# Performance work log

Hardware: AMD Instinct MI355X
Metric: run time of the kernel (lower is better)

## Reference

```python
import jax, jax.numpy as jnp
import numpy as np

C = 256   # num_channels
H = 16    # num_heads
L = 16384 # protein length
W = 15    # window (odd -> same-length conv with pad=(W-1)//2)


def setup_inputs() -> dict:
    key = jax.random.key(0)
    k = jax.random.split(key, 5)
    x = jax.random.normal(k[0], (1, C, L), dtype=jnp.float32)
    w_heads = jax.random.normal(k[1], (H, C, W), dtype=jnp.float32) * (1.0 / np.sqrt(C * W))
    b_heads = jax.random.normal(k[2], (H,), dtype=jnp.float32) * 0.01
    # grouped 1x1 conv with groups=H: per-head [C_out, C_in] matrices
    w_tr = jax.random.normal(k[3], (H, C, C), dtype=jnp.float32) * (1.0 / np.sqrt(C))
    b_tr = jax.random.normal(k[4], (H, C), dtype=jnp.float32) * 0.01
    return {"x": x, "w_heads": w_heads, "b_heads": b_heads, "w_tr": w_tr, "b_tr": b_tr}


def reference(x, w_heads, b_heads, w_tr, b_tr):
    pad = (W - 1) // 2
    # conv_heads: Conv1d(C -> H, kernel W, pad (W-1)//2)  -> scores [1, H, L]
    scores = jax.lax.conv_general_dilated(
        x, w_heads, window_strides=(1,), padding=[(pad, pad)],
        dimension_numbers=("NCH", "OIH", "NCH"),
    ) + b_heads[None, :, None]
    # batchwise softmax over sequence (single protein in batch -> softmax over L)
    focuses = jax.nn.softmax(scores, axis=-1)  # [1, H, L]
    # outer product: [1, H, 1, L] * [1, 1, C, L] -> [1, H, C, L] (the big intermediate)
    focused = focuses[:, :, None, :] * x[:, None, :, :]
    # grouped 1x1 conv (per-head CxC matmul) then sum over heads -> [1, C, L]
    out = jnp.einsum("hoc,bhcl->bol", w_tr, focused)
    out = out + jnp.sum(b_tr, axis=0)[None, :, None]  # head-summed per-group bias
    return out
```

## Files before the change

kernel.cpp:

```cpp
#include <hip/hip_runtime.h>
#include <hip/hip_bf16.h>

#define L_LEN 16384
#define C_CH  256
#define H_HEADS 16
#define W_WIN 15

typedef __attribute__((ext_vector_type(8))) short bf16x8;
typedef __attribute__((ext_vector_type(4))) float f32x4;
typedef unsigned short ushort_t;


__device__ __forceinline__ void gll16(const void* g, void* l) {
    __builtin_amdgcn_global_load_lds(
        (const __attribute__((address_space(1))) void*)g,
        (__attribute__((address_space(3))) void*)l, 16, 0, 0);
}

__device__ __forceinline__ ushort_t f2bf(float f) {
    __hip_bfloat16 b = __float2bfloat16(f);
    return *(ushort_t*)&b;
}

__global__ __launch_bounds__(256) void k_prep(const float* __restrict__ x,
                                              const float* __restrict__ wtr,
                                              const float* __restrict__ wh,
                                              ushort_t* __restrict__ xb,
                                              ushort_t* __restrict__ Ag,
                                              ushort_t* __restrict__ awf) {
    int bid = blockIdx.x;
    int t = threadIdx.x;
    if (bid < 1024) {
        __shared__ float tile[64][65];
        int l0 = (bid & 255) * 64;
        int c0 = (bid >> 8) * 64;
#pragma unroll
        for (int r = 0; r < 16; ++r) {
            int c = r * 4 + (t >> 6);
            int l = t & 63;
            tile[c][l] = x[(size_t)(c0 + c) * L_LEN + l0 + l];
        }
        __syncthreads();
        int l = t >> 2;
        int cq = (t & 3) * 16;
        ushort_t tmp[16];
#pragma unroll
        for (int i = 0; i < 16; ++i) tmp[i] = f2bf(tile[cq + i][l]);
        char* rowp = (char*)(xb + (size_t)(l0 + l) * C_CH);
        int swz = (l & 7) << 4;
        int b0 = (c0 + cq) * 2;
        *(uint4*)(rowp + (b0 ^ swz)) = *(uint4*)&tmp[0];
        *(uint4*)(rowp + ((b0 + 16) ^ swz)) = *(uint4*)&tmp[8];
    } else if (bid < 1536) {
        int tid = (bid - 1024) * 256 + t;
        size_t D = (size_t)tid * 16;
        int m = (int)(D >> 13);
        int inner = (int)(D & 8191);
        int kt = inner >> 7, wb = inner & 127;
        int ob = kt * 128 + (wb ^ ((m & 7) << 4));
        int k0 = ob >> 1;
        int h = k0 >> 8, c = k0 & 255;
        const float* src = wtr + ((size_t)h * C_CH + m) * C_CH + c;
        ushort_t tmp[8];
#pragma unroll
        for (int i = 0; i < 8; ++i) tmp[i] = f2bf(src[i]);
        *(uint4*)((char*)Ag + D) = *(uint4*)tmp;
    } else {
        int tid = (bid - 1536) * 256 + t;
        int e = tid & 7;
        int lane = (tid >> 3) & 63;
        int ktw = tid >> 9;
        int w = ktw >> 3, kt = ktw & 7;
        int h = lane & 15;
        int c = kt * 32 + (lane >> 4) * 8 + e;
        awf[tid] = f2bf(wh[((size_t)h * C_CH + c) * W_WIN + w]);
    }
}

__global__ __launch_bounds__(128) void k_convm(const ushort_t* __restrict__ xb,
                                               const ushort_t* __restrict__ awf,
                                               float* __restrict__ scores) {
    __shared__ char xs[48 * 512];
    int t = threadIdx.x;
    int n0 = blockIdx.x * 32;
#pragma unroll
    for (int i = 0; i < 12; ++i) {
        int chunk = t + i * 128;
        int rr = chunk >> 5;
        int cb = (chunk & 31) * 16;
        int l = n0 - 8 + rr;
        int lc = l < 0 ? 0 : (l >= L_LEN ? L_LEN - 1 : l);
        gll16((const char*)xb + (size_t)lc * 512 + cb, xs + chunk * 16);
    }
    __syncthreads();
    if (n0 == 0 || n0 == L_LEN - 32) {
        int rbase = (n0 == 0) ? 0 : 40;
        uint4 z = {0u, 0u, 0u, 0u};
#pragma unroll
        for (int i = 0; i < 2; ++i) {
            int ch = t + i * 128;
            *(uint4*)(xs + rbase * 512 + ch * 16) = z;
        }
        __syncthreads();
    }
    int wv = t >> 6, lane = t & 63;
    int r = lane & 15, q = lane >> 4;
    const f32x4 vzero = {0.f, 0.f, 0.f, 0.f};
    f32x4 acc[4] = {vzero, vzero, vzero, vzero};
    for (int w = 0; w < 15; ++w) {
        int rr = wv * 16 + r + w + 1;
        const char* rowp = &xs[rr * 512];
        int sw = (rr & 7) << 4;
#pragma unroll
        for (int kt = 0; kt < 8; ++kt) {
            bf16x8 a = *(const bf16x8*)(awf + (size_t)(((w * 8 + kt) * 64 + lane) * 8));
            bf16x8 b = *(const bf16x8*)(rowp + ((kt * 64 + q * 16) ^ sw));
            acc[kt & 3] = __builtin_amdgcn_mfma_f32_16x16x32_bf16(a, b, acc[kt & 3], 0, 0, 0);
        }
    }
    f32x4 s = acc[0] + acc[1] + acc[2] + acc[3];
    int nb = n0 + wv * 16;
#pragma unroll
    for (int e = 0; e < 4; ++e)
        scores[(size_t)(q * 4 + e) * L_LEN + nb + r] = s[e];
}

__global__ __launch_bounds__(1024) void k_stats(const float* __restrict__ scores,
                                                const float* __restrict__ btr,
                                                float2* __restrict__ MZ,
                                                float* __restrict__ bias) {
    int t = threadIdx.x;
    if (blockIdx.x == 16) {
        if (t < 256) {
            float s = 0.f;
#pragma unroll
            for (int h = 0; h < H_HEADS; ++h) s += btr[h * C_CH + t];
            bias[t] = s;
        }
        return;
    }
    __shared__ float red[17];
    int h = blockIdx.x;
    int wid = t >> 6, ln = t & 63;
    const float* sp = scores + (size_t)h * L_LEN;
    float v[16];
    float mx = -1e30f;
#pragma unroll
    for (int i = 0; i < 16; ++i) {
        v[i] = sp[i * 1024 + t];
        mx = fmaxf(mx, v[i]);
    }
    for (int o = 32; o > 0; o >>= 1) mx = fmaxf(mx, __shfl_xor(mx, o));
    if (ln == 0) red[wid] = mx;
    __syncthreads();
    if (t == 0) {
        float m2 = red[0];
        for (int i = 1; i < 16; ++i) m2 = fmaxf(m2, red[i]);
        red[16] = m2;
    }
    __syncthreads();
    float M = red[16];
    float s = 0.f;
#pragma unroll
    for (int i = 0; i < 16; ++i) s += __expf(v[i] - M);
    for (int o = 32; o > 0; o >>= 1) s += __shfl_xor(s, o);
    __syncthreads();
    if (ln == 0) red[wid] = s;
    __syncthreads();
    if (t == 0) {
        float Z = 0.f;
        for (int i = 0; i < 16; ++i) Z += red[i];
        float2 r; r.x = M; r.y = 1.0f / Z;
        MZ[h] = r;
    }
}

#define BRES 65536
#define ATS  16384
#define FTAB (BRES + 4 * ATS)

__global__ __launch_bounds__(512, 1) void k_gemm(const ushort_t* __restrict__ Ag,
                                                 const ushort_t* __restrict__ xb,
                                                 const float* __restrict__ scores,
                                                 const float2* __restrict__ MZ,
                                                 const float* __restrict__ bias,
                                                 float* __restrict__ out) {
    __shared__ char lds[FTAB + 8192];
    int t = threadIdx.x;
    int w = t >> 6, lane = t & 63;
    int m0 = blockIdx.y * 128, n0 = blockIdx.x * 128;
    int wr = w >> 2, wc = w & 3;
    int r = lane & 15, q = lane >> 4;
    int swz = (r & 7) << 4;

#pragma unroll
    for (int i = 0; i < 8; ++i) {
        int chunk = t + i * 512;
        int row = chunk >> 5, cb = (chunk & 31) * 16;
        gll16((const char*)xb + (size_t)(n0 + row) * 512 + cb, lds + chunk * 16);
    }
    {
        int idx = t * 4;
        int hh = idx >> 7, nn = idx & 127;
        float2 mz = MZ[hh];
        const float* sp = scores + (size_t)hh * L_LEN + n0 + nn;
        float* ft = (float*)(lds + FTAB);
#pragma unroll
        for (int e = 0; e < 4; ++e)
            ft[idx + e] = __expf(sp[e] - mz.x) * mz.y;
    }
    const f32x4 vzero = {0.f, 0.f, 0.f, 0.f};
    f32x4 oacc[4][2], hacc[4][2];
#pragma unroll
    for (int i = 0; i < 4; ++i)
#pragma unroll
        for (int j = 0; j < 2; ++j) { oacc[i][j] = vzero; hacc[i][j] = vzero; }

    bf16x8 br00_0, br00_1, br01_0, br01_1, br10_0, br10_1, br11_0, br11_1,
           br20_0, br20_1, br21_0, br21_1, br30_0, br30_1, br31_0, br31_1;

    __syncthreads();

    auto stageA = [&](int buf, int kt) {
        const char* src = (const char*)Ag + (size_t)(m0 + (t >> 3)) * 8192 + kt * 128 + (t & 7) * 16;
        char* dst = lds + BRES + buf * ATS + t * 16;
#pragma unroll
        for (int j = 0; j < 2; ++j)
            gll16(src + (size_t)j * 64 * 8192, dst + j * 8192);
    };

#define BRN(QQ, KK, J) br##QQ##KK##_##J
#define LDB(QQ, KK, J)                                                            \
    BRN(QQ, KK, J) = *(const bf16x8*)(lds + (wc * 32 + (J) * 16 + r) * 512 +      \
                          (((QQ) * 128 + (KK) * 64 + q * 16) ^ swz))
#define LDA_(Ab, I, KK)                                                           \
    (*(const bf16x8*)((Ab) + (wr * 64 + (I) * 16 + r) * 128 +                     \
                      (((KK) * 64 + q * 16) ^ swz)))
#define CK(Ab, KK, B0, B1)                                                        \
    {                                                                             \
        bf16x8 a0 = LDA_(Ab, 0, KK), a1 = LDA_(Ab, 1, KK),                        \
               a2 = LDA_(Ab, 2, KK), a3 = LDA_(Ab, 3, KK);                        \
        hacc[0][0] = __builtin_amdgcn_mfma_f32_16x16x32_bf16(a0, B0, hacc[0][0], 0, 0, 0); \
        hacc[0][1] = __builtin_amdgcn_mfma_f32_16x16x32_bf16(a0, B1, hacc[0][1], 0, 0, 0); \
        hacc[1][0] = __builtin_amdgcn_mfma_f32_16x16x32_bf16(a1, B0, hacc[1][0], 0, 0, 0); \
        hacc[1][1] = __builtin_amdgcn_mfma_f32_16x16x32_bf16(a1, B1, hacc[1][1], 0, 0, 0); \
        hacc[2][0] = __builtin_amdgcn_mfma_f32_16x16x32_bf16(a2, B0, hacc[2][0], 0, 0, 0); \
        hacc[2][1] = __builtin_amdgcn_mfma_f32_16x16x32_bf16(a2, B1, hacc[2][1], 0, 0, 0); \
        hacc[3][0] = __builtin_amdgcn_mfma_f32_16x16x32_bf16(a3, B0, hacc[3][0], 0, 0, 0); \
        hacc[3][1] = __builtin_amdgcn_mfma_f32_16x16x32_bf16(a3, B1, hacc[3][1], 0, 0, 0); \
    }
#define COMPUTE_LD(BUF, QQ)                                                       \
    {                                                                             \
        char* Ab = lds + BRES + (BUF) * ATS;                                      \
        __builtin_amdgcn_s_setprio(1);                                            \
        LDB(QQ, 0, 0); LDB(QQ, 0, 1);                                             \
        CK(Ab, 0, BRN(QQ, 0, 0), BRN(QQ, 0, 1));                                  \
        LDB(QQ, 1, 0); LDB(QQ, 1, 1);                                             \
        CK(Ab, 1, BRN(QQ, 1, 0), BRN(QQ, 1, 1));                                  \
        __builtin_amdgcn_s_setprio(0);                                            \
    }
#define COMPUTE_RE(BUF, QQ)                                                       \
    {                                                                             \
        char* Ab = lds + BRES + (BUF) * ATS;                                      \
        __builtin_amdgcn_s_setprio(1);                                            \
        CK(Ab, 0, BRN(QQ, 0, 0), BRN(QQ, 0, 1));                                  \
        CK(Ab, 1, BRN(QQ, 1, 0), BRN(QQ, 1, 1));                                  \
        __builtin_amdgcn_s_setprio(0);                                            \
    }
#define SCALE(H)                                                                  \
    {                                                                             \
        const float* ft = (const float*)(lds + FTAB) + (H) * 128;                 \
        float f0 = ft[wc * 32 + r], f1 = ft[wc * 32 + 16 + r];                    \
        _Pragma("unroll")                                                         \
        for (int i = 0; i < 4; ++i) {                                             \
            oacc[i][0] += hacc[i][0] * f0;                                        \
            oacc[i][1] += hacc[i][1] * f1;                                        \
            hacc[i][0] = vzero;                                                   \
            hacc[i][1] = vzero;                                                   \
        }                                                                         \
    }
#define PHASE(SBUF, SKT, CBUF, QQ, CMP)                                           \
    asm volatile("s_waitcnt vmcnt(4)" ::: "memory");                              \
    __builtin_amdgcn_s_barrier();                                                 \
    stageA((SBUF), (SKT));                                                        \
    CMP((CBUF), QQ);

    stageA(0, 0); stageA(1, 1); stageA(2, 2);

    PHASE(3, 3, 0, 0, COMPUTE_LD)
    PHASE(0, 4, 1, 1, COMPUTE_LD)
    PHASE(1, 5, 2, 2, COMPUTE_LD)
    PHASE(2, 6, 3, 3, COMPUTE_LD)
    SCALE(0);

    for (int h = 1; h < 15; ++h) {
        int k4 = h * 4;
        PHASE(3, k4 + 3, 0, 0, COMPUTE_RE)
        PHASE(0, k4 + 4, 1, 1, COMPUTE_RE)
        PHASE(1, k4 + 5, 2, 2, COMPUTE_RE)
        PHASE(2, k4 + 6, 3, 3, COMPUTE_RE)
        SCALE(h);
    }

    asm volatile("s_waitcnt vmcnt(4)" ::: "memory");
    __builtin_amdgcn_s_barrier();
    stageA(3, 63);
    COMPUTE_RE(0, 0);
    asm volatile("s_waitcnt vmcnt(4)" ::: "memory");
    __builtin_amdgcn_s_barrier();
    COMPUTE_RE(1, 1);
    asm volatile("s_waitcnt vmcnt(2)" ::: "memory");
    __builtin_amdgcn_s_barrier();
    COMPUTE_RE(2, 2);
    asm volatile("s_waitcnt vmcnt(0)" ::: "memory");
    __builtin_amdgcn_s_barrier();
    COMPUTE_RE(3, 3);
    SCALE(15);

#pragma unroll
    for (int i = 0; i < 4; ++i) {
        int mrow = m0 + wr * 64 + i * 16 + q * 4;
        float4 bv = *(const float4*)&bias[mrow];
        float bvr[4] = {bv.x, bv.y, bv.z, bv.w};
#pragma unroll
        for (int j = 0; j < 2; ++j) {
            int n = n0 + wc * 32 + j * 16 + r;
#pragma unroll
            for (int rr = 0; rr < 4; ++rr)
                out[(size_t)(mrow + rr) * L_LEN + n] = oacc[i][j][rr] + bvr[rr];
        }
    }
#undef PHASE
#undef SCALE
#undef COMPUTE_RE
#undef COMPUTE_LD
#undef CK
#undef LDA_
#undef LDB
#undef BRN
}

extern "C" void kernel_launch(void* const* d_in, const int* in_sizes, int n_in,
                              void* d_out, int out_size, void* d_ws, size_t ws_size,
                              hipStream_t stream) {
    const float* x   = (const float*)d_in[0];
    const float* wh  = (const float*)d_in[1];
    const float* wtr = (const float*)d_in[3];
    const float* btr = (const float*)d_in[4];
    float* out = (float*)d_out;
    char* ws = (char*)d_ws;

    ushort_t* Ag     = (ushort_t*)(ws);
    ushort_t* xb     = (ushort_t*)(ws + ((size_t)2 << 20));
    float*    scores = (float*)(ws + ((size_t)10 << 20));
    ushort_t* awf    = (ushort_t*)(ws + ((size_t)11 << 20));
    char*     sc     = ws + ((size_t)11 << 20) + (128 << 10);
    float2*   MZ     = (float2*)(sc);
    float*    bias   = (float*)(sc + 1024);

    k_prep<<<dim3(1776), 256, 0, stream>>>(x, wtr, wh, xb, Ag, awf);
    k_convm<<<dim3(512), 128, 0, stream>>>(xb, awf, scores);
    k_stats<<<dim3(17), 1024, 0, stream>>>(scores, btr, MZ, bias);
    k_gemm<<<dim3(128, 2), 512, 0, stream>>>(Ag, xb, scores, MZ, bias, out);
}
```

Measured before the change: 121.3 us.

## Drop stats kernel via atomic softmax denominators and widen GEMM A staging

After: 171.9 us. 41.7% more time.

```diff
diff --git a/kernel.cpp b/kernel.cpp
--- a/kernel.cpp
+++ b/kernel.cpp
@@ -25,9 +25,12 @@
 __global__ __launch_bounds__(256) void k_prep(const float* __restrict__ x,
                                               const float* __restrict__ wtr,
                                               const float* __restrict__ wh,
+                                              const float* __restrict__ btr,
                                               ushort_t* __restrict__ xb,
                                               ushort_t* __restrict__ Ag,
-                                              ushort_t* __restrict__ awf) {
+                                              ushort_t* __restrict__ awf,
+                                              float* __restrict__ bias,
+                                              float* __restrict__ Z) {
     int bid = blockIdx.x;
     int t = threadIdx.x;
     if (bid < 1024) {
@@ -65,7 +68,7 @@
 #pragma unroll
         for (int i = 0; i < 8; ++i) tmp[i] = f2bf(src[i]);
         *(uint4*)((char*)Ag + D) = *(uint4*)tmp;
-    } else {
+    } else if (bid < 1776) {
         int tid = (bid - 1536) * 256 + t;
         int e = tid & 7;
         int lane = (tid >> 3) & 63;
@@ -74,12 +77,19 @@
         int h = lane & 15;
         int c = kt * 32 + (lane >> 4) * 8 + e;
         awf[tid] = f2bf(wh[((size_t)h * C_CH + c) * W_WIN + w]);
+    } else {
+        float s = 0.f;
+#pragma unroll
+        for (int h = 0; h < H_HEADS; ++h) s += btr[h * C_CH + t];
+        bias[t] = s;
+        if (t < H_HEADS) Z[t] = 0.f;
     }
 }
 
 __global__ __launch_bounds__(128) void k_convm(const ushort_t* __restrict__ xb,
                                                const ushort_t* __restrict__ awf,
-                                               float* __restrict__ scores) {
+                                               float* __restrict__ scores,
+                                               float* __restrict__ Z) {
     __shared__ char xs[48 * 512];
     int t = threadIdx.x;
     int n0 = blockIdx.x * 32;
@@ -123,69 +133,31 @@
 #pragma unroll
     for (int e = 0; e < 4; ++e)
         scores[(size_t)(q * 4 + e) * L_LEN + nb + r] = s[e];
-}
-
-__global__ __launch_bounds__(1024) void k_stats(const float* __restrict__ scores,
-                                                const float* __restrict__ btr,
-                                                float2* __restrict__ MZ,
-                                                float* __restrict__ bias) {
-    int t = threadIdx.x;
-    if (blockIdx.x == 16) {
-        if (t < 256) {
-            float s = 0.f;
-#pragma unroll
-            for (int h = 0; h < H_HEADS; ++h) s += btr[h * C_CH + t];
-            bias[t] = s;
-        }
-        return;
-    }
-    __shared__ float red[17];
-    int h = blockIdx.x;
-    int wid = t >> 6, ln = t & 63;
-    const float* sp = scores + (size_t)h * L_LEN;
-    float v[16];
-    float mx = -1e30f;
-#pragma unroll
-    for (int i = 0; i < 16; ++i) {
-        v[i] = sp[i * 1024 + t];
-        mx = fmaxf(mx, v[i]);
-    }
-    for (int o = 32; o > 0; o >>= 1) mx = fmaxf(mx, __shfl_xor(mx, o));
-    if (ln == 0) red[wid] = mx;
-    __syncthreads();
-    if (t == 0) {
-        float m2 = red[0];
-        for (int i = 1; i < 16; ++i) m2 = fmaxf(m2, red[i]);
-        red[16] = m2;
-    }
-    __syncthreads();
-    float M = red[16];
-    float s = 0.f;
-#pragma unroll
-    for (int i = 0; i < 16; ++i) s += __expf(v[i] - M);
-    for (int o = 32; o > 0; o >>= 1) s += __shfl_xor(s, o);
-    __syncthreads();
-    if (ln == 0) red[wid] = s;
-    __syncthreads();
-    if (t == 0) {
-        float Z = 0.f;
-        for (int i = 0; i < 16; ++i) Z += red[i];
-        float2 r; r.x = M; r.y = 1.0f / Z;
-        MZ[h] = r;
-    }
-}
-
-#define BRES 65536
-#define ATS  16384
-#define FTAB (BRES + 4 * ATS)
+    f32x4 ez;
+#pragma unroll
+    for (int e = 0; e < 4; ++e) ez[e] = __expf(s[e]);
+#pragma unroll
+    for (int o = 1; o <= 8; o <<= 1) {
+#pragma unroll
+        for (int e = 0; e < 4; ++e) ez[e] += __shfl_xor(ez[e], o);
+    }
+    if (r == 0) {
+#pragma unroll
+        for (int e = 0; e < 4; ++e) atomicAdd(&Z[q * 4 + e], ez[e]);
+    }
+}
+
+#define BPAN 65536
+#define ATS2 32768
+#define FT   (BPAN + 2 * ATS2)
 
 __global__ __launch_bounds__(512, 1) void k_gemm(const ushort_t* __restrict__ Ag,
                                                  const ushort_t* __restrict__ xb,
                                                  const float* __restrict__ scores,
-                                                 const float2* __restrict__ MZ,
+                                                 const float* __restrict__ Z,
                                                  const float* __restrict__ bias,
                                                  float* __restrict__ out) {
-    __shared__ char lds[FTAB + 8192];
+    __shared__ char lds[FT + 8192];
     int t = threadIdx.x;
     int w = t >> 6, lane = t & 63;
     int m0 = blockIdx.y * 128, n0 = blockIdx.x * 128;
@@ -202,12 +174,12 @@
     {
         int idx = t * 4;
         int hh = idx >> 7, nn = idx & 127;
-        float2 mz = MZ[hh];
+        float invZ = 1.0f / Z[hh];
         const float* sp = scores + (size_t)hh * L_LEN + n0 + nn;
-        float* ft = (float*)(lds + FTAB);
+        float* ft = (float*)(lds + FT);
 #pragma unroll
         for (int e = 0; e < 4; ++e)
-            ft[idx + e] = __expf(sp[e] - mz.x) * mz.y;
+            ft[idx + e] = __expf(sp[e]) * invZ;
     }
     const f32x4 vzero = {0.f, 0.f, 0.f, 0.f};
     f32x4 oacc[4][2], hacc[4][2];
@@ -219,27 +191,34 @@
     bf16x8 br00_0, br00_1, br01_0, br01_1, br10_0, br10_1, br11_0, br11_1,
            br20_0, br20_1, br21_0, br21_1, br30_0, br30_1, br31_0, br31_1;
 
+    auto stageT = [&](int buf, int T) {
+        int base = (t >> 6) * 4096;
+        int loff = (t & 63) * 16;
+        char* dst = lds + BPAN + buf * ATS2;
+        const char* src = (const char*)Ag + (size_t)T * 256;
+#pragma unroll
+        for (int j = 0; j < 4; ++j) {
+            int lin = base + j * 1024 + loff;
+            int row = lin >> 8, col = lin & 255;
+            gll16(src + (size_t)(m0 + row) * 8192 + col, dst + lin);
+        }
+    };
+
+    stageT(0, 0);
     __syncthreads();
-
-    auto stageA = [&](int buf, int kt) {
-        const char* src = (const char*)Ag + (size_t)(m0 + (t >> 3)) * 8192 + kt * 128 + (t & 7) * 16;
-        char* dst = lds + BRES + buf * ATS + t * 16;
-#pragma unroll
-        for (int j = 0; j < 2; ++j)
-            gll16(src + (size_t)j * 64 * 8192, dst + j * 8192);
-    };
 
 #define BRN(QQ, KK, J) br##QQ##KK##_##J
 #define LDB(QQ, KK, J)                                                            \
     BRN(QQ, KK, J) = *(const bf16x8*)(lds + (wc * 32 + (J) * 16 + r) * 512 +      \
-                          (((QQ) * 128 + (KK) * 64 + q * 16) ^ swz))
-#define LDA_(Ab, I, KK)                                                           \
-    (*(const bf16x8*)((Ab) + (wr * 64 + (I) * 16 + r) * 128 +                     \
+                          (((QQ) * 128 + (KK) * 64 + q * 16) ^ swz));
+#define LDBN(QQ, KK, J)
+#define LDA2(Ab, I, KK, P)                                                        \
+    (*(const bf16x8*)((Ab) + (wr * 64 + (I) * 16 + r) * 256 + (P) * 128 +         \
                       (((KK) * 64 + q * 16) ^ swz)))
-#define CK(Ab, KK, B0, B1)                                                        \
+#define CKP(Ab, P, KK, B0, B1)                                                    \
     {                                                                             \
-        bf16x8 a0 = LDA_(Ab, 0, KK), a1 = LDA_(Ab, 1, KK),                        \
-               a2 = LDA_(Ab, 2, KK), a3 = LDA_(Ab, 3, KK);                        \
+        bf16x8 a0 = LDA2(Ab, 0, KK, P), a1 = LDA2(Ab, 1, KK, P),                  \
+               a2 = LDA2(Ab, 2, KK, P), a3 = LDA2(Ab, 3, KK, P);                  \
         hacc[0][0] = __builtin_amdgcn_mfma_f32_16x16x32_bf16(a0, B0, hacc[0][0], 0, 0, 0); \
         hacc[0][1] = __builtin_amdgcn_mfma_f32_16x16x32_bf16(a0, B1, hacc[0][1], 0, 0, 0); \
         hacc[1][0] = __builtin_amdgcn_mfma_f32_16x16x32_bf16(a1, B0, hacc[1][0], 0, 0, 0); \
@@ -249,27 +228,23 @@
         hacc[3][0] = __builtin_amdgcn_mfma_f32_16x16x32_bf16(a3, B0, hacc[3][0], 0, 0, 0); \
         hacc[3][1] = __builtin_amdgcn_mfma_f32_16x16x32_bf16(a3, B1, hacc[3][1], 0, 0, 0); \
     }
-#define COMPUTE_LD(BUF, QQ)                                                       \
+#define PHASE(BUF, Q0, Q1, LM)                                                    \
     {                                                                             \
-        char* Ab = lds + BRES + (BUF) * ATS;                                      \
+        char* Ab = lds + BPAN + (BUF) * ATS2;                                     \
         __builtin_amdgcn_s_setprio(1);                                            \
-        LDB(QQ, 0, 0); LDB(QQ, 0, 1);                                             \
-        CK(Ab, 0, BRN(QQ, 0, 0), BRN(QQ, 0, 1));                                  \
-        LDB(QQ, 1, 0); LDB(QQ, 1, 1);                                             \
-        CK(Ab, 1, BRN(QQ, 1, 0), BRN(QQ, 1, 1));                                  \
-        __builtin_amdgcn_s_setprio(0);                                            \
-    }
-#define COMPUTE_RE(BUF, QQ)                                                       \
-    {                                                                             \
-        char* Ab = lds + BRES + (BUF) * ATS;                                      \
-        __builtin_amdgcn_s_setprio(1);                                            \
-        CK(Ab, 0, BRN(QQ, 0, 0), BRN(QQ, 0, 1));                                  \
-        CK(Ab, 1, BRN(QQ, 1, 0), BRN(QQ, 1, 1));                                  \
+        LM(Q0, 0, 0) LM(Q0, 0, 1)                                                 \
+        CKP(Ab, 0, 0, BRN(Q0, 0, 0), BRN(Q0, 0, 1))                               \
+        LM(Q0, 1, 0) LM(Q0, 1, 1)                                                 \
+        CKP(Ab, 0, 1, BRN(Q0, 1, 0), BRN(Q0, 1, 1))                               \
+        LM(Q1, 0, 0) LM(Q1, 0, 1)                                                 \
+        CKP(Ab, 1, 0, BRN(Q1, 0, 0), BRN(Q1, 0, 1))                               \
+        LM(Q1, 1, 0) LM(Q1, 1, 1)                                                 \
+        CKP(Ab, 1, 1, BRN(Q1, 1, 0), BRN(Q1, 1, 1))                               \
         __builtin_amdgcn_s_setprio(0);                                            \
     }
 #define SCALE(H)                                                                  \
     {                                                                             \
-        const float* ft = (const float*)(lds + FTAB) + (H) * 128;                 \
+        const float* ft = (const float*)(lds + FT) + (H) * 128;                   \
         float f0 = ft[wc * 32 + r], f1 = ft[wc * 32 + 16 + r];                    \
         _Pragma("unroll")                                                         \
         for (int i = 0; i < 4; ++i) {                                             \
@@ -279,42 +254,29 @@
             hacc[i][1] = vzero;                                                   \
         }                                                                         \
     }
-#define PHASE(SBUF, SKT, CBUF, QQ, CMP)                                           \
-    asm volatile("s_waitcnt vmcnt(4)" ::: "memory");                              \
-    __builtin_amdgcn_s_barrier();                                                 \
-    stageA((SBUF), (SKT));                                                        \
-    CMP((CBUF), QQ);
-
-    stageA(0, 0); stageA(1, 1); stageA(2, 2);
-
-    PHASE(3, 3, 0, 0, COMPUTE_LD)
-    PHASE(0, 4, 1, 1, COMPUTE_LD)
-    PHASE(1, 5, 2, 2, COMPUTE_LD)
-    PHASE(2, 6, 3, 3, COMPUTE_LD)
+#define WB asm volatile("s_waitcnt vmcnt(0)" ::: "memory"); __builtin_amdgcn_s_barrier();
+
+    stageT(1, 1);
+    PHASE(0, 0, 1, LDB)
+    WB
+    stageT(0, 2);
+    PHASE(1, 2, 3, LDB)
     SCALE(0);
 
     for (int h = 1; h < 15; ++h) {
-        int k4 = h * 4;
-        PHASE(3, k4 + 3, 0, 0, COMPUTE_RE)
-        PHASE(0, k4 + 4, 1, 1, COMPUTE_RE)
-        PHASE(1, k4 + 5, 2, 2, COMPUTE_RE)
-        PHASE(2, k4 + 6, 3, 3, COMPUTE_RE)
+        WB
+        stageT(1, 2 * h + 1);
+        PHASE(0, 0, 1, LDBN)
+        WB
+        stageT(0, 2 * h + 2);
+        PHASE(1, 2, 3, LDBN)
         SCALE(h);
     }
-
-    asm volatile("s_waitcnt vmcnt(4)" ::: "memory");
-    __builtin_amdgcn_s_barrier();
-    stageA(3, 63);
-    COMPUTE_RE(0, 0);
-    asm volatile("s_waitcnt vmcnt(4)" ::: "memory");
-    __builtin_amdgcn_s_barrier();
-    COMPUTE_RE(1, 1);
-    asm volatile("s_waitcnt vmcnt(2)" ::: "memory");
-    __builtin_amdgcn_s_barrier();
-    COMPUTE_RE(2, 2);
-    asm volatile("s_waitcnt vmcnt(0)" ::: "memory");
-    __builtin_amdgcn_s_barrier();
-    COMPUTE_RE(3, 3);
+    WB
+    stageT(1, 31);
+    PHASE(0, 0, 1, LDBN)
+    WB
+    PHASE(1, 2, 3, LDBN)
     SCALE(15);
 
 #pragma unroll
@@ -330,12 +292,12 @@
                 out[(size_t)(mrow + rr) * L_LEN + n] = oacc[i][j][rr] + bvr[rr];
         }
     }
+#undef WB
+#undef SCALE
 #undef PHASE
-#undef SCALE
-#undef COMPUTE_RE
-#undef COMPUTE_LD
-#undef CK
-#undef LDA_
+#undef CKP
+#undef LDA2
+#undef LDBN
 #undef LDB
 #undef BRN
 }
@@ -355,11 +317,10 @@
     float*    scores = (float*)(ws + ((size_t)10 << 20));
     ushort_t* awf    = (ushort_t*)(ws + ((size_t)11 << 20));
     char*     sc     = ws + ((size_t)11 << 20) + (128 << 10);
-    float2*   MZ     = (float2*)(sc);
+    float*    Z      = (float*)(sc);
     float*    bias   = (float*)(sc + 1024);
 
-    k_prep<<<dim3(1776), 256, 0, stream>>>(x, wtr, wh, xb, Ag, awf);
-    k_convm<<<dim3(512), 128, 0, stream>>>(xb, awf, scores);
-    k_stats<<<dim3(17), 1024, 0, stream>>>(scores, btr, MZ, bias);
-    k_gemm<<<dim3(128, 2), 512, 0, stream>>>(Ag, xb, scores, MZ, bias, out);
-}
+    k_prep<<<dim3(1777), 256, 0, stream>>>(x, wtr, wh, btr, xb, Ag, awf, bias, Z);
+    k_convm<<<dim3(512), 128, 0, stream>>>(xb, awf, scores, Z);
+    k_gemm<<<dim3(128, 2), 512, 0, stream>>>(Ag, xb, scores, Z, bias, out);
+}
```

## Fuse softmax denominator into conv via atomics and drop stats kernel

Applied to the files above, without the earlier changes.

Result: slower. 140.8 us (+16.0%).

```diff
diff --git a/kernel.cpp b/kernel.cpp
--- a/kernel.cpp
+++ b/kernel.cpp
@@ -25,9 +25,12 @@
 __global__ __launch_bounds__(256) void k_prep(const float* __restrict__ x,
                                               const float* __restrict__ wtr,
                                               const float* __restrict__ wh,
+                                              const float* __restrict__ btr,
                                               ushort_t* __restrict__ xb,
                                               ushort_t* __restrict__ Ag,
-                                              ushort_t* __restrict__ awf) {
+                                              ushort_t* __restrict__ awf,
+                                              float* __restrict__ bias,
+                                              float* __restrict__ Z) {
     int bid = blockIdx.x;
     int t = threadIdx.x;
     if (bid < 1024) {
@@ -65,7 +68,7 @@
 #pragma unroll
         for (int i = 0; i < 8; ++i) tmp[i] = f2bf(src[i]);
         *(uint4*)((char*)Ag + D) = *(uint4*)tmp;
-    } else {
+    } else if (bid < 1776) {
         int tid = (bid - 1536) * 256 + t;
         int e = tid & 7;
         int lane = (tid >> 3) & 63;
@@ -74,33 +77,45 @@
         int h = lane & 15;
         int c = kt * 32 + (lane >> 4) * 8 + e;
         awf[tid] = f2bf(wh[((size_t)h * C_CH + c) * W_WIN + w]);
-    }
-}
-
-__global__ __launch_bounds__(128) void k_convm(const ushort_t* __restrict__ xb,
+    } else {
+        float s = 0.f;
+#pragma unroll
+        for (int h = 0; h < H_HEADS; ++h) s += btr[h * C_CH + t];
+        bias[t] = s;
+        Z[t] = 0.f;
+    }
+}
+
+#define CV_XS 122880
+__global__ __launch_bounds__(256) void k_convm(const ushort_t* __restrict__ xb,
                                                const ushort_t* __restrict__ awf,
-                                               float* __restrict__ scores) {
-    __shared__ char xs[48 * 512];
+                                               float* __restrict__ scores,
+                                               float* __restrict__ Z) {
+    __shared__ char sm[CV_XS + 79 * 512];
     int t = threadIdx.x;
-    int n0 = blockIdx.x * 32;
-#pragma unroll
-    for (int i = 0; i < 12; ++i) {
-        int chunk = t + i * 128;
-        int rr = chunk >> 5;
-        int cb = (chunk & 31) * 16;
-        int l = n0 - 8 + rr;
-        int lc = l < 0 ? 0 : (l >= L_LEN ? L_LEN - 1 : l);
-        gll16((const char*)xb + (size_t)lc * 512 + cb, xs + chunk * 16);
+    int n0 = blockIdx.x * 64;
+#pragma unroll
+    for (int i = 0; i < 30; ++i) {
+        int chunk = t + i * 256;
+        gll16((const char*)awf + (size_t)chunk * 16, sm + chunk * 16);
+    }
+    for (int i = 0; i < 10; ++i) {
+        int chunk = t + i * 256;
+        if (chunk < 79 * 32) {
+            int rr = chunk >> 5, cb = (chunk & 31) * 16;
+            int l = n0 - 8 + rr;
+            int lc = l < 0 ? 0 : (l >= L_LEN ? L_LEN - 1 : l);
+            gll16((const char*)xb + (size_t)lc * 512 + cb, sm + CV_XS + chunk * 16);
+        }
     }
     __syncthreads();
-    if (n0 == 0 || n0 == L_LEN - 32) {
-        int rbase = (n0 == 0) ? 0 : 40;
-        uint4 z = {0u, 0u, 0u, 0u};
-#pragma unroll
-        for (int i = 0; i < 2; ++i) {
-            int ch = t + i * 128;
-            *(uint4*)(xs + rbase * 512 + ch * 16) = z;
-        }
+    if (n0 == 0) {
+        uint4 zz = {0u, 0u, 0u, 0u};
+        *(uint4*)(sm + CV_XS + t * 16) = zz;
+        __syncthreads();
+    } else if (n0 == L_LEN - 64) {
+        uint4 zz = {0u, 0u, 0u, 0u};
+        if (t < 224) *(uint4*)(sm + CV_XS + 72 * 512 + t * 16) = zz;
         __syncthreads();
     }
     int wv = t >> 6, lane = t & 63;
@@ -109,11 +124,11 @@
     f32x4 acc[4] = {vzero, vzero, vzero, vzero};
     for (int w = 0; w < 15; ++w) {
         int rr = wv * 16 + r + w + 1;
-        const char* rowp = &xs[rr * 512];
+        const char* rowp = sm + CV_XS + rr * 512;
         int sw = (rr & 7) << 4;
 #pragma unroll
         for (int kt = 0; kt < 8; ++kt) {
-            bf16x8 a = *(const bf16x8*)(awf + (size_t)(((w * 8 + kt) * 64 + lane) * 8));
+            bf16x8 a = *(const bf16x8*)(sm + ((w * 8 + kt) * 64 + lane) * 16);
             bf16x8 b = *(const bf16x8*)(rowp + ((kt * 64 + q * 16) ^ sw));
             acc[kt & 3] = __builtin_amdgcn_mfma_f32_16x16x32_bf16(a, b, acc[kt & 3], 0, 0, 0);
         }
@@ -123,55 +138,17 @@
 #pragma unroll
     for (int e = 0; e < 4; ++e)
         scores[(size_t)(q * 4 + e) * L_LEN + nb + r] = s[e];
-}
-
-__global__ __launch_bounds__(1024) void k_stats(const float* __restrict__ scores,
-                                                const float* __restrict__ btr,
-                                                float2* __restrict__ MZ,
-                                                float* __restrict__ bias) {
-    int t = threadIdx.x;
-    if (blockIdx.x == 16) {
-        if (t < 256) {
-            float s = 0.f;
-#pragma unroll
-            for (int h = 0; h < H_HEADS; ++h) s += btr[h * C_CH + t];
-            bias[t] = s;
-        }
-        return;
-    }
-    __shared__ float red[17];
-    int h = blockIdx.x;
-    int wid = t >> 6, ln = t & 63;
-    const float* sp = scores + (size_t)h * L_LEN;
-    float v[16];
-    float mx = -1e30f;
-#pragma unroll
-    for (int i = 0; i < 16; ++i) {
-        v[i] = sp[i * 1024 + t];
-        mx = fmaxf(mx, v[i]);
-    }
-    for (int o = 32; o > 0; o >>= 1) mx = fmaxf(mx, __shfl_xor(mx, o));
-    if (ln == 0) red[wid] = mx;
-    __syncthreads();
-    if (t == 0) {
-        float m2 = red[0];
-        for (int i = 1; i < 16; ++i) m2 = fmaxf(m2, red[i]);
-        red[16] = m2;
-    }
-    __syncthreads();
-    float M = red[16];
-    float s = 0.f;
-#pragma unroll
-    for (int i = 0; i < 16; ++i) s += __expf(v[i] - M);
-    for (int o = 32; o > 0; o >>= 1) s += __shfl_xor(s, o);
-    __syncthreads();
-    if (ln == 0) red[wid] = s;
-    __syncthreads();
-    if (t == 0) {
-        float Z = 0.f;
-        for (int i = 0; i < 16; ++i) Z += red[i];
-        float2 r; r.x = M; r.y = 1.0f / Z;
-        MZ[h] = r;
+    f32x4 ez;
+#pragma unroll
+    for (int e = 0; e < 4; ++e) ez[e] = __expf(s[e]);
+#pragma unroll
+    for (int o = 1; o <= 8; o <<= 1) {
+#pragma unroll
+        for (int e = 0; e < 4; ++e) ez[e] += __shfl_xor(ez[e], o);
+    }
+    if (r == 0) {
+#pragma unroll
+        for (int e = 0; e < 4; ++e) atomicAdd(&Z[(q * 4 + e) * 16], ez[e]);
     }
 }
 
@@ -182,7 +159,7 @@
 __global__ __launch_bounds__(512, 1) void k_gemm(const ushort_t* __restrict__ Ag,
                                                  const ushort_t* __restrict__ xb,
                                                  const float* __restrict__ scores,
-                                                 const float2* __restrict__ MZ,
+                                                 const float* __restrict__ Z,
                                                  const float* __restrict__ bias,
                                                  float* __restrict__ out) {
     __shared__ char lds[FTAB + 8192];
@@ -202,12 +179,12 @@
     {
         int idx = t * 4;
         int hh = idx >> 7, nn = idx & 127;
-        float2 mz = MZ[hh];
+        float invZ = 1.0f / Z[hh * 16];
         const float* sp = scores + (size_t)hh * L_LEN + n0 + nn;
         float* ft = (float*)(lds + FTAB);
 #pragma unroll
         for (int e = 0; e < 4; ++e)
-            ft[idx + e] = __expf(sp[e] - mz.x) * mz.y;
+            ft[idx + e] = __expf(sp[e]) * invZ;
     }
     const f32x4 vzero = {0.f, 0.f, 0.f, 0.f};
     f32x4 oacc[4][2], hacc[4][2];
@@ -355,11 +332,10 @@
     float*    scores = (float*)(ws + ((size_t)10 << 20));
     ushort_t* awf    = (ushort_t*)(ws + ((size_t)11 << 20));
     char*     sc     = ws + ((size_t)11 << 20) + (128 << 10);
-    float2*   MZ     = (float2*)(sc);
+    float*    Z      = (float*)(sc);
     float*    bias   = (float*)(sc + 1024);
 
-    k_prep<<<dim3(1776), 256, 0, stream>>>(x, wtr, wh, xb, Ag, awf);
-    k_convm<<<dim3(512), 128, 0, stream>>>(xb, awf, scores);
-    k_stats<<<dim3(17), 1024, 0, stream>>>(scores, btr, MZ, bias);
-    k_gemm<<<dim3(128, 2), 512, 0, stream>>>(Ag, xb, scores, MZ, bias, out);
-}
+    k_prep<<<dim3(1777), 256, 0, stream>>>(x, wtr, wh, btr, xb, Ag, awf, bias, Z);
+    k_convm<<<dim3(256), 256, 0, stream>>>(xb, awf, scores, Z);
+    k_gemm<<<dim3(128, 2), 512, 0, stream>>>(Ag, xb, scores, Z, bias, out);
+}
```
